# Optimization experiments

Measured on AMD Instinct MI355X. Metric: run time of the kernel, lower is better.

## Reference

```python
import jax, jax.numpy as jnp
import numpy as np

B, T, D, H = 512, 64, 16, 1024  # H must equal T*D (required by the original reshape)


def setup_inputs() -> dict:
    key = jax.random.key(0)
    ks = list(jax.random.split(key, 30))
    def nrm(k, shape, s=0.05):
        return jax.random.normal(k, shape, dtype=jnp.float32) * s
    inp = {}
    inp["values"] = jax.random.normal(ks[0], (B, T, D), dtype=jnp.float32)
    inp["masks"] = (jax.random.uniform(ks[1], (B, T, D)) < 0.8).astype(jnp.float32)
    i = 2
    for pre in ("fw", "bw"):
        for l, din in ((0, D), (1, H)):
            inp[f"{pre}_Wih{l}"] = nrm(ks[i], (4 * H, din)); i += 1
            inp[f"{pre}_Whh{l}"] = nrm(ks[i], (4 * H, H)); i += 1
            inp[f"{pre}_bih{l}"] = nrm(ks[i], (4 * H,)); i += 1
            inp[f"{pre}_bhh{l}"] = nrm(ks[i], (4 * H,)); i += 1
    inp["out_W"] = nrm(ks[i], (D, H)); i += 1
    inp["out_b"] = nrm(ks[i], (D,)); i += 1
    inp["fcb_W"] = nrm(ks[i], (D, 1)); i += 1
    inp["fcb_b"] = nrm(ks[i], (D,)); i += 1
    inp["fce_W"] = nrm(ks[i], (D, 1)); i += 1
    inp["fce_b"] = nrm(ks[i], (D,)); i += 1
    return inp


def _lstm_cell(x, h, c, Wih, Whh, bih, bhh):
    # PyTorch LSTMCell: gate order i, f, g, o
    gates = x @ Wih.T + bih + h @ Whh.T + bhh
    i, f, g, o = jnp.split(gates, 4, axis=-1)
    c2 = jax.nn.sigmoid(f) * c + jax.nn.sigmoid(i) * jnp.tanh(g)
    return jax.nn.sigmoid(o) * jnp.tanh(c2), c2


def _forward(values, masks, fw_Wih0, fw_Whh0, fw_bih0, fw_bhh0, fw_Wih1, fw_Whh1, fw_bih1, fw_bhh1,
             bw_Wih0, bw_Whh0, bw_bih0, bw_bhh0, bw_Wih1, bw_Whh1, bw_bih1, bw_bhh1,
             out_W, out_b, fcb_W, fcb_b, fce_W, fce_b):
    Bc, Tc, Dc = values.shape
    zeros = jnp.zeros((Bc, H), values.dtype)
    bwd_values = jnp.flip(values, 1)
    bwd_masks = jnp.flip(masks, 1)
    # fc_begin/fc_end outputs are dead code in the original (init loop starts at layer 1)
    # Original pre-loop: layers 1..L-1 run once with zero inputs/states.
    hf1, cf1 = _lstm_cell(zeros, zeros, zeros, fw_Wih1, fw_Whh1, fw_bih1, fw_bhh1)
    hb1, cb1 = _lstm_cell(zeros, zeros, zeros, bw_Wih1, bw_Whh1, bw_bih1, bw_bhh1)
    carry0 = (zeros, zeros, hf1, cf1, zeros, zeros, hb1, cb1)

    def step(carry, xs):
        hf0, cf0, hf1, cf1, hb0, cb0, hb1, cb1 = carry
        x_f, m_f, x_b, m_b = xs
        cc_f = (1.0 - m_f) * (hf1 @ out_W.T + out_b) + m_f * x_f
        cc_b = (1.0 - m_b) * (hb1 @ out_W.T + out_b) + m_b * x_b
        hf0, cf0 = _lstm_cell(cc_f, hf0, cf0, fw_Wih0, fw_Whh0, fw_bih0, fw_bhh0)
        hf1, cf1 = _lstm_cell(hf0, hf1, cf1, fw_Wih1, fw_Whh1, fw_bih1, fw_bhh1)
        hb0, cb0 = _lstm_cell(cc_b, hb0, cb0, bw_Wih0, bw_Whh0, bw_bih0, bw_bhh0)
        hb1, cb1 = _lstm_cell(hb0, hb1, cb1, bw_Wih1, bw_Whh1, bw_bih1, bw_bhh1)
        return (hf0, cf0, hf1, cf1, hb0, cb0, hb1, cb1), None

    xs = (jnp.swapaxes(values, 0, 1), jnp.swapaxes(masks, 0, 1),
          jnp.swapaxes(bwd_values, 0, 1), jnp.swapaxes(bwd_masks, 0, 1))
    carry, _ = jax.lax.scan(step, carry0, xs)
    hf1, hb1 = carry[2], carry[6]
    # Original averages fwd with hidden-dim-flipped bwd hidden state
    h = (hf1 + jnp.flip(hb1, 1)) * 0.5
    imputations = h.reshape(Bc, Tc, Dc)
    imputed = imputations * (1.0 - masks) + values * masks
    return h, imputations, imputed


def reference(values, masks, fw_Wih0, fw_Whh0, fw_bih0, fw_bhh0, fw_Wih1, fw_Whh1, fw_bih1, fw_bhh1,
              bw_Wih0, bw_Whh0, bw_bih0, bw_bhh0, bw_Wih1, bw_Whh1, bw_bih1, bw_bhh1,
              out_W, out_b, fcb_W, fcb_b, fce_W, fce_b):
    return _forward(values, masks, fw_Wih0, fw_Whh0, fw_bih0, fw_bhh0, fw_Wih1, fw_Whh1, fw_bih1, fw_bhh1,
                    bw_Wih0, bw_Whh0, bw_bih0, bw_bhh0, bw_Wih1, bw_Whh1, bw_bih1, bw_bhh1,
                    out_W, out_b, fcb_W, fcb_b, fce_W, fce_b)
```

## Files before the change

### kernel.cpp

```cpp
#include <hip/hip_runtime.h>
#include <cstdint>
#include <cstddef>

typedef unsigned short u16;
typedef __attribute__((ext_vector_type(8))) short short8;
typedef __attribute__((ext_vector_type(4))) short short4v;
typedef __attribute__((ext_vector_type(4))) float f32x4;

#define NB 512
#define NT 64
#define ND 16
#define NH 1024

#define WAITV(N) asm volatile("s_waitcnt vmcnt(" #N ")" ::: "memory")
#define BARR __builtin_amdgcn_s_barrier(); __builtin_amdgcn_sched_barrier(0)

__device__ __forceinline__ u16 f2bf(float x) {
  union { float f; unsigned u; } v; v.f = x;
  unsigned r = v.u + 0x7fffu + ((v.u >> 16) & 1u);
  return (u16)(r >> 16);
}
__device__ __forceinline__ float bf2f(u16 u) {
  union { float f; unsigned u; } v; v.u = ((unsigned)u) << 16;
  return v.f;
}
__device__ __forceinline__ float sigf(float x) { return 1.f / (1.f + __expf(-x)); }

__device__ __forceinline__ void glds16(const void* g, void* l) {
  __builtin_amdgcn_global_load_lds((const __attribute__((address_space(1))) void*)g,
                                   (__attribute__((address_space(3))) void*)l, 16, 0, 0);
}

__device__ __forceinline__ int swz(int row, int col) {
  return ((((col >> 3) ^ (row & 7)) << 3) | (col & 7));
}

__device__ __forceinline__ int inv_np(int np) {
  int hb = np >> 6, g = (np >> 4) & 3, hlo = np & 15;
  return g * 1024 + hb * 16 + hlo;
}

__global__ void k_prep_big(const float* s0, const float* s1, const float* s2,
                           const float* s3, const float* s4, const float* s5, u16* dst) {
  for (unsigned q = blockIdx.x * 256 + threadIdx.x; q < (6u << 20); q += gridDim.x * 256) {
    int mat = q >> 20;
    int rem = q & ((1 << 20) - 1);
    int np = rem >> 8;
    int k = (rem & 255) * 4;
    int row = inv_np(np);
    const float* s = mat == 0 ? s0 : mat == 1 ? s1 : mat == 2 ? s2 : mat == 3 ? s3 : mat == 4 ? s4 : s5;
    float4 v = *(const float4*)(s + (size_t)row * NH + k);
    u16* d = dst + (size_t)mat * 4194304 + (size_t)np * NH + swz(np, k);
    d[0] = f2bf(v.x); d[1] = f2bf(v.y); d[2] = f2bf(v.z); d[3] = f2bf(v.w);
  }
}

__global__ void k_prep_small(const float* fwih0, const float* bwih0,
                             const float* fbi0, const float* fbh0, const float* fbi1, const float* fbh1,
                             const float* bbi0, const float* bbh0, const float* bbi1, const float* bbh1,
                             const float* outW,
                             u16* wih0p, float* biasb, u16* owbf) {
  int idx = blockIdx.x * 256 + threadIdx.x;
  if (idx < 524288) {
    int dir = idx >> 18;
    int r = idx & 262143;
    int np = r >> 6, d = r & 63;
    int row = inv_np(np);
    const float* s = dir ? bwih0 : fwih0;
    float v = (d < 16) ? s[row * 16 + d] : 0.f;
    wih0p[(size_t)dir * 262144 + (size_t)np * 64 + swz(np, d)] = f2bf(v);
  } else if (idx < 524288 + 16384) {
    int j = idx - 524288;
    int which = j >> 12;
    int np = j & 4095;
    int row = inv_np(np);
    const float* bi = which == 0 ? fbi0 : which == 1 ? fbi1 : which == 2 ? bbi0 : bbi1;
    const float* bh = which == 0 ? fbh0 : which == 1 ? fbh1 : which == 2 ? bbh0 : bbh1;
    biasb[which * 4096 + np] = bi[row] + bh[row];
  } else if (idx < 524288 + 16384 + 16384) {
    int j = idx - 524288 - 16384;
    owbf[j] = f2bf(outW[j]);
  }
}

__global__ void k_init(const float* fbi1, const float* fbh1, const float* bbi1, const float* bbh1,
                       float* c0, float* c1, u16* h0bf, u16* h1bf) {
  int idx = blockIdx.x * 256 + threadIdx.x;
  int dir = idx >> 19;
  int rem = idx & ((1 << 19) - 1);
  int b = rem >> 10, h = rem & 1023;
  const float* bi = dir ? bbi1 : fbi1;
  const float* bh = dir ? bbh1 : fbh1;
  float gi = bi[h] + bh[h];
  float gg = bi[2048 + h] + bh[2048 + h];
  float go = bi[3072 + h] + bh[3072 + h];
  float c = sigf(gi) * tanhf(gg);
  float hv = sigf(go) * tanhf(c);
  size_t o = (size_t)dir * 524288 + rem;
  c1[o] = c;
  h1bf[(size_t)(dir * 2) * 524288 + (size_t)b * NH + swz(b, h)] = f2bf(hv);
  c0[o] = 0.f;
  h0bf[(size_t)(dir * 2) * 524288 + rem] = 0;
}

__global__ __launch_bounds__(256) void k_cc0(const u16* h1f, const u16* h1b,
                                             const float* outW, float* partial) {
  int dir = blockIdx.y;
  int w = threadIdx.x >> 6, lane = threadIdx.x & 63;
  int b = blockIdx.x * 4 + w;
  const u16* hb = dir ? h1b : h1f;
  int key = b & 7;
  short8 ha = *(const short8*)(hb + (size_t)b * NH + ((lane * 2) ^ key) * 8);
  short8 hc = *(const short8*)(hb + (size_t)b * NH + ((lane * 2 + 1) ^ key) * 8);
  float hf[16];
#pragma unroll
  for (int j = 0; j < 8; ++j) { hf[j] = bf2f((u16)ha[j]); hf[8 + j] = bf2f((u16)hc[j]); }
  float sums[16];
#pragma unroll
  for (int d = 0; d < 16; ++d) {
    const float* wr = outW + (size_t)d * NH + lane * 16;
    float s = 0.f;
#pragma unroll
    for (int j = 0; j < 16; ++j) s += hf[j] * wr[j];
#pragma unroll
    for (int off = 32; off; off >>= 1) s += __shfl_xor(s, off);
    sums[d] = s;
  }
  if (lane == 0) {
    float* dst = partial + (size_t)dir * 524288 + (size_t)b * 16;
#pragma unroll
    for (int d = 0; d < 16; ++d) dst[d] = sums[d];
  }
}

struct AF { short8 a[4]; };

struct StepCtx {
  u16* h0bf; u16* h1bf;
  const u16* wbig; const u16* wih0p;
  const float* biasb;
  float* c0; float* c1;
  float* partial;
  const float* values; const float* masks; const float* outb;
  const u16* owbf;
};

__global__ __launch_bounds__(256, 2) void k_g0(StepCtx a, int t) {
  __shared__ u16 SM[3 * 8192 + 4096];
  const int dir = blockIdx.z, m_blk = blockIdx.y, n_blk = blockIdx.x;
  const int p = t & 1;
  const int m0 = m_blk * 64, n0 = n_blk * 128;
  const int tid = threadIdx.x, w = tid >> 6, lane = tid & 63;
  const int srow = lane >> 3, scol = (lane & 7) * 8;
  const int wm = w >> 1, wn = w & 1;
  const int fr = lane & 15, fq = lane >> 4, key = fr & 7;
  const u16* h0_in = a.h0bf + (size_t)(dir * 2 + p) * 524288;
  u16* h0_out = a.h0bf + (size_t)(dir * 2 + 1 - p) * 524288;
  const u16* W00 = a.wbig + (size_t)(dir * 3 + 0) * 4194304;
  const u16* Wcc = a.wih0p + (size_t)dir * 262144;
  const float* bias0 = a.biasb + (size_t)dir * 2 * 4096;
  float* cs0 = a.c0 + (size_t)dir * 524288;
  const u16* hA = h0_in + (size_t)m0 * NH;
  u16* SMX = SM + 3 * 8192;

  int aoffg[4], aoffs[4], boff[8];
#pragma unroll
  for (int mi = 0; mi < 2; ++mi)
#pragma unroll
    for (int kk = 0; kk < 2; ++kk) {
      aoffg[mi * 2 + kk] = (wm * 32 + mi * 16 + fr) * NH + ((fq + kk * 4) ^ key) * 8;
      aoffs[mi * 2 + kk] = (wm * 32 + mi * 16 + fr) * 64 + ((fq + kk * 4) ^ key) * 8;
    }
#pragma unroll
  for (int ni = 0; ni < 4; ++ni)
#pragma unroll
    for (int kk = 0; kk < 2; ++kk)
      boff[ni * 2 + kk] = (wn * 64 + ni * 16 + fr) * 64 + ((fq + kk * 4) ^ key) * 8;

  f32x4 acc[2][4];
#pragma unroll
  for (int i = 0; i < 2; ++i)
#pragma unroll
    for (int j = 0; j < 4; ++j) acc[i][j] = f32x4{0.f, 0.f, 0.f, 0.f};

  auto stageB = [&](int c, int buf) {
    u16* lb = SM + buf * 8192;
    const u16* pw = W00 + (size_t)(c - 1) * 64;
#pragma unroll
    for (int k = 0; k < 4; ++k)
      glds16(pw + (size_t)(n0 + w * 32 + k * 8 + srow) * NH + scol, lb + (w * 32 + k * 8) * 64);
  };
  auto ldA = [&](int c, AF& F) {
    const u16* pa = hA + (size_t)(c - 1) * 64;
#pragma unroll
    for (int i = 0; i < 4; ++i) F.a[i] = *(const short8*)(pa + aoffg[i]);
  };
  auto comp = [&](int buf, const AF& F) {
    const u16* base = SM + buf * 8192;
#pragma unroll
    for (int ni = 0; ni < 4; ++ni)
#pragma unroll
      for (int kk = 0; kk < 2; ++kk) {
        short8 bfrag = *(const short8*)(base + boff[ni * 2 + kk]);
#pragma unroll
        for (int mi = 0; mi < 2; ++mi)
          acc[mi][ni] = __builtin_amdgcn_mfma_f32_16x16x32_bf16(F.a[mi * 2 + kk], bfrag, acc[mi][ni], 0, 0, 0);
      }
  };

  AF Aa, Ab, Ac;
#pragma unroll
  for (int k = 0; k < 4; ++k)
    glds16(Wcc + (size_t)(n0 + w * 32 + k * 8 + srow) * 64 + scol, SM + (w * 32 + k * 8) * 64);
  stageB(1, 1); ldA(1, Ab);
  __builtin_amdgcn_sched_barrier(0);

  {
    const int rl = tid >> 2, q = tid & 3;
    const int grow = m0 + rl;
    const int d4 = q * 4;
    float4 ps0 = {0.f, 0.f, 0.f, 0.f}, ps1 = {0.f, 0.f, 0.f, 0.f};
    const float* pp = a.partial + (size_t)dir * 524288 + (size_t)grow * 16 + d4;
#pragma unroll 4
    for (int nb = 0; nb < 64; nb += 2) {
      float4 v0 = *(const float4*)(pp + (size_t)nb * 8192);
      float4 v1 = *(const float4*)(pp + (size_t)(nb + 1) * 8192);
      ps0.x += v0.x; ps0.y += v0.y; ps0.z += v0.z; ps0.w += v0.w;
      ps1.x += v1.x; ps1.y += v1.y; ps1.z += v1.z; ps1.w += v1.w;
    }
    float4 ps = {ps0.x + ps1.x, ps0.y + ps1.y, ps0.z + ps1.z, ps0.w + ps1.w};
    int tt = dir ? (NT - 1 - t) : t;
    float4 x = *(const float4*)(a.values + ((size_t)grow * NT + tt) * ND + d4);
    float4 m = *(const float4*)(a.masks + ((size_t)grow * NT + tt) * ND + d4);
    float4 ob = *(const float4*)(a.outb + d4);
    short4v cc;
    cc[0] = (short)f2bf((1.f - m.x) * (ps.x + ob.x) + m.x * x.x);
    cc[1] = (short)f2bf((1.f - m.y) * (ps.y + ob.y) + m.y * x.y);
    cc[2] = (short)f2bf((1.f - m.z) * (ps.z + ob.z) + m.z * x.z);
    cc[3] = (short)f2bf((1.f - m.w) * (ps.w + ob.w) + m.w * x.w);
    int k2 = rl & 7;
    *(short4v*)(SMX + rl * 64 + (((d4 >> 3) ^ k2) << 3) + (d4 & 7)) = cc;
    short8 z8 = {0, 0, 0, 0, 0, 0, 0, 0};
    *(short8*)(SMX + rl * 64 + (((2 + q) ^ k2) << 3)) = z8;
    if (q < 2) *(short8*)(SMX + rl * 64 + (((6 + q) ^ k2) << 3)) = z8;
    asm volatile("s_waitcnt lgkmcnt(0)" ::: "memory");
    __builtin_amdgcn_sched_barrier(0);
  }

  WAITV(8); BARR;
  stageB(2, 2); ldA(2, Ac);
  {
    AF F0;
#pragma unroll
    for (int i = 0; i < 4; ++i) F0.a[i] = *(const short8*)(SMX + aoffs[i]);
    comp(0, F0);
  }
  WAITV(8); BARR; stageB(3, 0); ldA(3, Aa); comp(1, Ab);
  for (int c = 2; c < 14; c += 3) {
    WAITV(8); BARR; stageB(c + 2, 1); ldA(c + 2, Ab); comp(2, Ac);
    WAITV(8); BARR; stageB(c + 3, 2); ldA(c + 3, Ac); comp(0, Aa);
    WAITV(8); BARR; stageB(c + 4, 0); ldA(c + 4, Aa); comp(1, Ab);
  }
  WAITV(8); BARR; stageB(16, 1); ldA(16, Ab); comp(2, Ac);
  WAITV(8); BARR; comp(0, Aa);
  WAITV(0); BARR; comp(1, Ab);

  const int hg = ((n0 + wn * 64) >> 2) + fr;
  const float b0 = bias0[n0 + wn * 64 + fr];
  const float b1 = bias0[n0 + wn * 64 + 16 + fr];
  const float b2 = bias0[n0 + wn * 64 + 32 + fr];
  const float b3 = bias0[n0 + wn * 64 + 48 + fr];
#pragma unroll
  for (int mi = 0; mi < 2; ++mi)
#pragma unroll
    for (int r = 0; r < 4; ++r) {
      int row = m0 + wm * 32 + mi * 16 + fq * 4 + r;
      size_t sidx = (size_t)row * NH + hg;
      float iv = acc[mi][0][r] + b0;
      float fv = acc[mi][1][r] + b1;
      float gv = acc[mi][2][r] + b2;
      float ov = acc[mi][3][r] + b3;
      float cp = cs0[sidx];
      float c2 = sigf(fv) * cp + sigf(iv) * tanhf(gv);
      float hvv = sigf(ov) * tanhf(c2);
      cs0[sidx] = c2;
      h0_out[(size_t)row * NH + swz(row, hg)] = f2bf(hvv);
    }
}

__global__ __launch_bounds__(256, 2) void k_g1(StepCtx a, int t) {
  __shared__ u16 SM[3 * 8192];
  const int dir = blockIdx.z, m_blk = blockIdx.y, n_blk = blockIdx.x;
  const int p = t & 1;
  const int m0 = m_blk * 64, n0 = n_blk * 128;
  const int tid = threadIdx.x, w = tid >> 6, lane = tid & 63;
  const int srow = lane >> 3, scol = (lane & 7) * 8;
  const int wm = w >> 1, wn = w & 1;
  const int fr = lane & 15, fq = lane >> 4, key = fr & 7;
  const u16* h0_new = a.h0bf + (size_t)(dir * 2 + 1 - p) * 524288;
  const u16* h1_in = a.h1bf + (size_t)(dir * 2 + p) * 524288;
  u16* h1_out = a.h1bf + (size_t)(dir * 2 + 1 - p) * 524288;
  const u16* W10 = a.wbig + (size_t)(dir * 3 + 1) * 4194304;
  const u16* W11 = a.wbig + (size_t)(dir * 3 + 2) * 4194304;
  const float* bias1 = a.biasb + (size_t)(dir * 2 + 1) * 4096;
  float* cs1 = a.c1 + (size_t)dir * 524288;
  const u16* hA0 = h0_new + (size_t)m0 * NH;
  const u16* hA1 = h1_in + (size_t)m0 * NH;

  int aoffg[4], boff[8];
#pragma unroll
  for (int mi = 0; mi < 2; ++mi)
#pragma unroll
    for (int kk = 0; kk < 2; ++kk)
      aoffg[mi * 2 + kk] = (wm * 32 + mi * 16 + fr) * NH + ((fq + kk * 4) ^ key) * 8;
#pragma unroll
  for (int ni = 0; ni < 4; ++ni)
#pragma unroll
    for (int kk = 0; kk < 2; ++kk)
      boff[ni * 2 + kk] = (wn * 64 + ni * 16 + fr) * 64 + ((fq + kk * 4) ^ key) * 8;

  f32x4 acc[2][4];
#pragma unroll
  for (int i = 0; i < 2; ++i)
#pragma unroll
    for (int j = 0; j < 4; ++j) acc[i][j] = f32x4{0.f, 0.f, 0.f, 0.f};

  auto stageB = [&](int c, int buf) {
    u16* lb = SM + buf * 8192;
    const u16* pw = (c < 16) ? (W10 + (size_t)c * 64) : (W11 + (size_t)(c - 16) * 64);
#pragma unroll
    for (int k = 0; k < 4; ++k)
      glds16(pw + (size_t)(n0 + w * 32 + k * 8 + srow) * NH + scol, lb + (w * 32 + k * 8) * 64);
  };
  auto ldA = [&](int c, AF& F) {
    const u16* pa = (c < 16) ? (hA0 + (size_t)c * 64) : (hA1 + (size_t)(c - 16) * 64);
#pragma unroll
    for (int i = 0; i < 4; ++i) F.a[i] = *(const short8*)(pa + aoffg[i]);
  };
  auto comp = [&](int buf, const AF& F) {
    const u16* base = SM + buf * 8192;
#pragma unroll
    for (int ni = 0; ni < 4; ++ni)
#pragma unroll
      for (int kk = 0; kk < 2; ++kk) {
        short8 bfrag = *(const short8*)(base + boff[ni * 2 + kk]);
#pragma unroll
        for (int mi = 0; mi < 2; ++mi)
          acc[mi][ni] = __builtin_amdgcn_mfma_f32_16x16x32_bf16(F.a[mi * 2 + kk], bfrag, acc[mi][ni], 0, 0, 0);
      }
  };

  AF Aa, Ab, Ac;
  stageB(0, 0); ldA(0, Aa);
  stageB(1, 1); ldA(1, Ab);
  __builtin_amdgcn_sched_barrier(0);

  for (int c = 0; c < 30; c += 3) {
    WAITV(8); BARR; stageB(c + 2, 2); ldA(c + 2, Ac); comp(0, Aa);
    WAITV(8); BARR; stageB(c + 3, 0); ldA(c + 3, Aa); comp(1, Ab);
    WAITV(8); BARR; stageB(c + 4, 1); ldA(c + 4, Ab); comp(2, Ac);
  }
  WAITV(8); BARR; comp(0, Aa);
  WAITV(0); BARR; comp(1, Ab);

  const int hb4 = (n0 + wn * 64) >> 2;
  const int hg = hb4 + fr;
  const float b0 = bias1[n0 + wn * 64 + fr];
  const float b1 = bias1[n0 + wn * 64 + 16 + fr];
  const float b2 = bias1[n0 + wn * 64 + 32 + fr];
  const float b3 = bias1[n0 + wn * 64 + 48 + fr];
  float hsv[2][4];
#pragma unroll
  for (int mi = 0; mi < 2; ++mi)
#pragma unroll
    for (int r = 0; r < 4; ++r) {
      int row = m0 + wm * 32 + mi * 16 + fq * 4 + r;
      size_t sidx = (size_t)row * NH + hg;
      float iv = acc[mi][0][r] + b0;
      float fv = acc[mi][1][r] + b1;
      float gv = acc[mi][2][r] + b2;
      float ov = acc[mi][3][r] + b3;
      float cp = cs1[sidx];
      float c2 = sigf(fv) * cp + sigf(iv) * tanhf(gv);
      float hvv = sigf(ov) * tanhf(c2);
      cs1[sidx] = c2;
      h1_out[(size_t)row * NH + swz(row, hg)] = f2bf(hvv);
      hsv[mi][r] = hvv;
    }

  {
    u16* ts = SM + w * 512;
    *(short4v*)(ts + (lane >> 2) * 32 + 16 + (lane & 3) * 4) = short4v{0, 0, 0, 0};
    short8 afr = {0, 0, 0, 0, 0, 0, 0, 0};
    if (fq < 2) afr = *(const short8*)(a.owbf + (size_t)fr * NH + hb4 + fq * 8);
    float* pout = a.partial + ((size_t)(dir * 64 + n_blk * 2 + wn) * 512) * 16;
#pragma unroll
    for (int mi = 0; mi < 2; ++mi) {
#pragma unroll
      for (int r = 0; r < 4; ++r)
        *(ts + (fq * 4 + r) * 32 + fr) = f2bf(hsv[mi][r]);
      asm volatile("s_waitcnt lgkmcnt(0)" ::: "memory");
      __builtin_amdgcn_sched_barrier(0);
      short8 bfr2 = *(const short8*)(ts + fr * 32 + fq * 8);
      f32x4 pz = {0.f, 0.f, 0.f, 0.f};
      pz = __builtin_amdgcn_mfma_f32_16x16x32_bf16(afr, bfr2, pz, 0, 0, 0);
      int row = m0 + wm * 32 + mi * 16 + fr;
      float4 st = {pz[0], pz[1], pz[2], pz[3]};
      *(float4*)(pout + (size_t)row * 16 + fq * 4) = st;
      asm volatile("s_waitcnt lgkmcnt(0)" ::: "memory");
      __builtin_amdgcn_sched_barrier(0);
    }
  }
}

__global__ void k_final(const u16* hf1, const u16* hb1, const float* values,
                        const float* masks, float* out) {
  int idx = blockIdx.x * 256 + threadIdx.x;
  int b = idx >> 10, j = idx & 1023;
  float hf = bf2f(hf1[(size_t)b * NH + swz(b, j)]);
  int jr = NH - 1 - j;
  float hb = bf2f(hb1[(size_t)b * NH + swz(b, jr)]);
  float hv = 0.5f * (hf + hb);
  float m = masks[idx];
  out[idx] = hv;
  out[524288 + idx] = hv;
  out[1048576 + idx] = hv * (1.f - m) + values[idx] * m;
}

extern "C" void kernel_launch(void* const* d_in, const int* in_sizes, int n_in,
                              void* d_out, int out_size, void* d_ws, size_t ws_size,
                              hipStream_t stream) {
  const float* values  = (const float*)d_in[0];
  const float* masks   = (const float*)d_in[1];
  const float* fw_Wih0 = (const float*)d_in[2];
  const float* fw_Whh0 = (const float*)d_in[3];
  const float* fw_bih0 = (const float*)d_in[4];
  const float* fw_bhh0 = (const float*)d_in[5];
  const float* fw_Wih1 = (const float*)d_in[6];
  const float* fw_Whh1 = (const float*)d_in[7];
  const float* fw_bih1 = (const float*)d_in[8];
  const float* fw_bhh1 = (const float*)d_in[9];
  const float* bw_Wih0 = (const float*)d_in[10];
  const float* bw_Whh0 = (const float*)d_in[11];
  const float* bw_bih0 = (const float*)d_in[12];
  const float* bw_bhh0 = (const float*)d_in[13];
  const float* bw_Wih1 = (const float*)d_in[14];
  const float* bw_Whh1 = (const float*)d_in[15];
  const float* bw_bih1 = (const float*)d_in[16];
  const float* bw_bhh1 = (const float*)d_in[17];
  const float* out_W   = (const float*)d_in[18];
  const float* out_b   = (const float*)d_in[19];

  char* ws = (char*)d_ws;
  u16* wbig    = (u16*)ws;
  u16* wih0p   = (u16*)(ws + 50331648);
  float* biasb = (float*)(ws + 51380224);
  u16* owbf    = (u16*)(ws + 51445760);
  float* c0    = (float*)(ws + 51478528);
  float* c1    = (float*)(ws + 55672832);
  u16* h0bf    = (u16*)(ws + 59867136);
  u16* h1bf    = (u16*)(ws + 64061440);
  float* partial = (float*)(ws + 68255744);
  if (ws_size < 72450048) return;

  k_prep_big<<<4096, 256, 0, stream>>>(fw_Whh0, fw_Wih1, fw_Whh1, bw_Whh0, bw_Wih1, bw_Whh1, wbig);
  k_prep_small<<<2176, 256, 0, stream>>>(fw_Wih0, bw_Wih0, fw_bih0, fw_bhh0, fw_bih1, fw_bhh1,
                                         bw_bih0, bw_bhh0, bw_bih1, bw_bhh1, out_W,
                                         wih0p, biasb, owbf);
  k_init<<<4096, 256, 0, stream>>>(fw_bih1, fw_bhh1, bw_bih1, bw_bhh1, c0, c1, h0bf, h1bf);
  hipMemsetAsync(partial, 0, 4194304, stream);
  k_cc0<<<dim3(128, 2), 256, 0, stream>>>(h1bf, h1bf + (size_t)2 * 524288, out_W, partial);

  StepCtx sc;
  sc.h0bf = h0bf; sc.h1bf = h1bf;
  sc.wbig = wbig; sc.wih0p = wih0p;
  sc.biasb = biasb; sc.c0 = c0; sc.c1 = c1;
  sc.partial = partial;
  sc.values = values; sc.masks = masks; sc.outb = out_b;
  sc.owbf = owbf;

  for (int t = 0; t < NT; ++t) {
    k_g0<<<dim3(32, 8, 2), 256, 0, stream>>>(sc, t);
    k_g1<<<dim3(32, 8, 2), 256, 0, stream>>>(sc, t);
  }

  k_final<<<2048, 256, 0, stream>>>(h1bf, h1bf + (size_t)2 * 524288, values, masks, (float*)d_out);
}
```

Measured before the change: 3.268 ms.

## Recompute output projection in g0 via MFMA instead of partial sums from g1

Drops the per-tile partial output-projection epilogue in k_g1, the partial buffer, its memset and the k_cc0 init kernel. Instead, k_g0 computes the full 16-wide projection of the previous layer-1 hidden state directly with 32 MFMA steps over the bf16 h1 row and out_W. This removes the 64-way partial-sum read and write traffic and shortens g1, at the cost of redundant projection work in every g0 block (each n-block recomputes it). It also forces a full vmcnt(0) wait before the first barrier, which may reduce overlap with the prefetched weight loads.

```diff
diff --git a/kernel.cpp b/kernel.cpp
--- a/kernel.cpp
+++ b/kernel.cpp
@@ -103,36 +103,6 @@
   h0bf[(size_t)(dir * 2) * 524288 + rem] = 0;
 }
 
-__global__ __launch_bounds__(256) void k_cc0(const u16* h1f, const u16* h1b,
-                                             const float* outW, float* partial) {
-  int dir = blockIdx.y;
-  int w = threadIdx.x >> 6, lane = threadIdx.x & 63;
-  int b = blockIdx.x * 4 + w;
-  const u16* hb = dir ? h1b : h1f;
-  int key = b & 7;
-  short8 ha = *(const short8*)(hb + (size_t)b * NH + ((lane * 2) ^ key) * 8);
-  short8 hc = *(const short8*)(hb + (size_t)b * NH + ((lane * 2 + 1) ^ key) * 8);
-  float hf[16];
-#pragma unroll
-  for (int j = 0; j < 8; ++j) { hf[j] = bf2f((u16)ha[j]); hf[8 + j] = bf2f((u16)hc[j]); }
-  float sums[16];
-#pragma unroll
-  for (int d = 0; d < 16; ++d) {
-    const float* wr = outW + (size_t)d * NH + lane * 16;
-    float s = 0.f;
-#pragma unroll
-    for (int j = 0; j < 16; ++j) s += hf[j] * wr[j];
-#pragma unroll
-    for (int off = 32; off; off >>= 1) s += __shfl_xor(s, off);
-    sums[d] = s;
-  }
-  if (lane == 0) {
-    float* dst = partial + (size_t)dir * 524288 + (size_t)b * 16;
-#pragma unroll
-    for (int d = 0; d < 16; ++d) dst[d] = sums[d];
-  }
-}
-
 struct AF { short8 a[4]; };
 
 struct StepCtx {
@@ -140,7 +110,6 @@
   const u16* wbig; const u16* wih0p;
   const float* biasb;
   float* c0; float* c1;
-  float* partial;
   const float* values; const float* masks; const float* outb;
   const u16* owbf;
 };
@@ -156,6 +125,7 @@
   const int fr = lane & 15, fq = lane >> 4, key = fr & 7;
   const u16* h0_in = a.h0bf + (size_t)(dir * 2 + p) * 524288;
   u16* h0_out = a.h0bf + (size_t)(dir * 2 + 1 - p) * 524288;
+  const u16* h1_in = a.h1bf + (size_t)(dir * 2 + p) * 524288;
   const u16* W00 = a.wbig + (size_t)(dir * 3 + 0) * 4194304;
   const u16* Wcc = a.wih0p + (size_t)dir * 262144;
   const float* bias0 = a.biasb + (size_t)dir * 2 * 4096;
@@ -216,38 +186,39 @@
   __builtin_amdgcn_sched_barrier(0);
 
   {
-    const int rl = tid >> 2, q = tid & 3;
-    const int grow = m0 + rl;
-    const int d4 = q * 4;
-    float4 ps0 = {0.f, 0.f, 0.f, 0.f}, ps1 = {0.f, 0.f, 0.f, 0.f};
-    const float* pp = a.partial + (size_t)dir * 524288 + (size_t)grow * 16 + d4;
-#pragma unroll 4
-    for (int nb = 0; nb < 64; nb += 2) {
-      float4 v0 = *(const float4*)(pp + (size_t)nb * 8192);
-      float4 v1 = *(const float4*)(pp + (size_t)(nb + 1) * 8192);
-      ps0.x += v0.x; ps0.y += v0.y; ps0.z += v0.z; ps0.w += v0.w;
-      ps1.x += v1.x; ps1.y += v1.y; ps1.z += v1.z; ps1.w += v1.w;
+    const int lrow = fr;
+    const int kgrp = fq;
+    const int rowg = m0 + w * 16 + lrow;
+    const int keyr = rowg & 7;
+    const u16* hrow = h1_in + (size_t)rowg * NH;
+    const u16* owr = a.owbf + (size_t)lrow * NH + kgrp * 8;
+    f32x4 ccacc = {0.f, 0.f, 0.f, 0.f};
+#pragma unroll
+    for (int kc = 0; kc < 32; ++kc) {
+      short8 bfh = *(const short8*)(hrow + (((kc * 4 + kgrp) ^ keyr) << 3));
+      short8 afo = *(const short8*)(owr + kc * 32);
+      ccacc = __builtin_amdgcn_mfma_f32_16x16x32_bf16(afo, bfh, ccacc, 0, 0, 0);
     }
-    float4 ps = {ps0.x + ps1.x, ps0.y + ps1.y, ps0.z + ps1.z, ps0.w + ps1.w};
     int tt = dir ? (NT - 1 - t) : t;
-    float4 x = *(const float4*)(a.values + ((size_t)grow * NT + tt) * ND + d4);
-    float4 m = *(const float4*)(a.masks + ((size_t)grow * NT + tt) * ND + d4);
-    float4 ob = *(const float4*)(a.outb + d4);
+    float4 x = *(const float4*)(a.values + ((size_t)rowg * NT + tt) * ND + kgrp * 4);
+    float4 m = *(const float4*)(a.masks + ((size_t)rowg * NT + tt) * ND + kgrp * 4);
+    float4 ob = *(const float4*)(a.outb + kgrp * 4);
     short4v cc;
-    cc[0] = (short)f2bf((1.f - m.x) * (ps.x + ob.x) + m.x * x.x);
-    cc[1] = (short)f2bf((1.f - m.y) * (ps.y + ob.y) + m.y * x.y);
-    cc[2] = (short)f2bf((1.f - m.z) * (ps.z + ob.z) + m.z * x.z);
-    cc[3] = (short)f2bf((1.f - m.w) * (ps.w + ob.w) + m.w * x.w);
-    int k2 = rl & 7;
-    *(short4v*)(SMX + rl * 64 + (((d4 >> 3) ^ k2) << 3) + (d4 & 7)) = cc;
+    cc[0] = (short)f2bf((1.f - m.x) * (ccacc[0] + ob.x) + m.x * x.x);
+    cc[1] = (short)f2bf((1.f - m.y) * (ccacc[1] + ob.y) + m.y * x.y);
+    cc[2] = (short)f2bf((1.f - m.z) * (ccacc[2] + ob.z) + m.z * x.z);
+    cc[3] = (short)f2bf((1.f - m.w) * (ccacc[3] + ob.w) + m.w * x.w);
+    const int rl = w * 16 + lrow;
+    const int k2 = rl & 7;
+    *(short4v*)(SMX + rl * 64 + (((kgrp >> 1) ^ k2) << 3) + (kgrp & 1) * 4) = cc;
     short8 z8 = {0, 0, 0, 0, 0, 0, 0, 0};
-    *(short8*)(SMX + rl * 64 + (((2 + q) ^ k2) << 3)) = z8;
-    if (q < 2) *(short8*)(SMX + rl * 64 + (((6 + q) ^ k2) << 3)) = z8;
+    *(short8*)(SMX + rl * 64 + (((2 + kgrp) ^ k2) << 3)) = z8;
+    if (kgrp < 2) *(short8*)(SMX + rl * 64 + (((6 + kgrp) ^ k2) << 3)) = z8;
     asm volatile("s_waitcnt lgkmcnt(0)" ::: "memory");
     __builtin_amdgcn_sched_barrier(0);
   }
 
-  WAITV(8); BARR;
+  WAITV(0); BARR;
   stageB(2, 2); ldA(2, Ac);
   {
     AF F0;
@@ -369,7 +340,6 @@
   const float b1 = bias1[n0 + wn * 64 + 16 + fr];
   const float b2 = bias1[n0 + wn * 64 + 32 + fr];
   const float b3 = bias1[n0 + wn * 64 + 48 + fr];
-  float hsv[2][4];
 #pragma unroll
   for (int mi = 0; mi < 2; ++mi)
 #pragma unroll
@@ -385,32 +355,7 @@
       float hvv = sigf(ov) * tanhf(c2);
       cs1[sidx] = c2;
       h1_out[(size_t)row * NH + swz(row, hg)] = f2bf(hvv);
-      hsv[mi][r] = hvv;
     }
-
-  {
-    u16* ts = SM + w * 512;
-    *(short4v*)(ts + (lane >> 2) * 32 + 16 + (lane & 3) * 4) = short4v{0, 0, 0, 0};
-    short8 afr = {0, 0, 0, 0, 0, 0, 0, 0};
-    if (fq < 2) afr = *(const short8*)(a.owbf + (size_t)fr * NH + hb4 + fq * 8);
-    float* pout = a.partial + ((size_t)(dir * 64 + n_blk * 2 + wn) * 512) * 16;
-#pragma unroll
-    for (int mi = 0; mi < 2; ++mi) {
-#pragma unroll
-      for (int r = 0; r < 4; ++r)
-        *(ts + (fq * 4 + r) * 32 + fr) = f2bf(hsv[mi][r]);
-      asm volatile("s_waitcnt lgkmcnt(0)" ::: "memory");
-      __builtin_amdgcn_sched_barrier(0);
-      short8 bfr2 = *(const short8*)(ts + fr * 32 + fq * 8);
-      f32x4 pz = {0.f, 0.f, 0.f, 0.f};
-      pz = __builtin_amdgcn_mfma_f32_16x16x32_bf16(afr, bfr2, pz, 0, 0, 0);
-      int row = m0 + wm * 32 + mi * 16 + fr;
-      float4 st = {pz[0], pz[1], pz[2], pz[3]};
-      *(float4*)(pout + (size_t)row * 16 + fq * 4) = st;
-      asm volatile("s_waitcnt lgkmcnt(0)" ::: "memory");
-      __builtin_amdgcn_sched_barrier(0);
-    }
-  }
 }
 
 __global__ void k_final(const u16* hf1, const u16* hb1, const float* values,
@@ -460,22 +405,18 @@
   float* c1    = (float*)(ws + 55672832);
   u16* h0bf    = (u16*)(ws + 59867136);
   u16* h1bf    = (u16*)(ws + 64061440);
-  float* partial = (float*)(ws + 68255744);
-  if (ws_size < 72450048) return;
+  if (ws_size < 68255744) return;
 
   k_prep_big<<<4096, 256, 0, stream>>>(fw_Whh0, fw_Wih1, fw_Whh1, bw_Whh0, bw_Wih1, bw_Whh1, wbig);
   k_prep_small<<<2176, 256, 0, stream>>>(fw_Wih0, bw_Wih0, fw_bih0, fw_bhh0, fw_bih1, fw_bhh1,
                                          bw_bih0, bw_bhh0, bw_bih1, bw_bhh1, out_W,
                                          wih0p, biasb, owbf);
   k_init<<<4096, 256, 0, stream>>>(fw_bih1, fw_bhh1, bw_bih1, bw_bhh1, c0, c1, h0bf, h1bf);
-  hipMemsetAsync(partial, 0, 4194304, stream);
-  k_cc0<<<dim3(128, 2), 256, 0, stream>>>(h1bf, h1bf + (size_t)2 * 524288, out_W, partial);
 
   StepCtx sc;
   sc.h0bf = h0bf; sc.h1bf = h1bf;
   sc.wbig = wbig; sc.wih0p = wih0p;
   sc.biasb = biasb; sc.c0 = c0; sc.c1 = c1;
-  sc.partial = partial;
   sc.values = values; sc.masks = masks; sc.outb = out_b;
   sc.owbf = owbf;
 
```

After: 3.430 ms. 1.05x slower.
